# Performance work log

Measured on AMD Instinct MI355X. Metric: run time of the kernel, lower is better.

## Reference

```python
import jax, jax.numpy as jnp
import numpy as np

N_NODES = 8192
IN_F = 256
OUT_F = 256
ALPHA = 0.2  # LeakyReLU negative slope


def setup_inputs() -> dict:
    key = jax.random.key(0)
    k1, k2, k3, k4 = jax.random.split(key, 4)
    X = jax.random.normal(k1, (N_NODES, IN_F), dtype=jnp.float32)
    A = jax.random.randint(k2, (N_NODES, N_NODES), 0, 2, dtype=jnp.int32)
    # torch nn.Linear weight layout: (out_features, in_features)
    W = jax.random.normal(k3, (OUT_F, IN_F), dtype=jnp.float32) * (1.0 / np.sqrt(IN_F))
    r = jax.random.normal(k4, (2 * OUT_F, 1), dtype=jnp.float32)
    return {"X": X, "A": A, "W": W, "r": r}


def reference(X, A, W, r):
    # Wh = X @ W^T  -> (N, F_out)
    Wh = X @ W.T
    # Split r so that cat([Wh_i, Wh_j]) @ r == Wh_i @ r_src + Wh_j @ r_dst
    F_out = Wh.shape[-1]
    r_src = r[:F_out, 0]   # (F,)
    r_dst = r[F_out:, 0]   # (F,)
    s_i = Wh @ r_src       # (N,)
    s_j = Wh @ r_dst       # (N,)
    e = s_i[:, None] + s_j[None, :]                      # (N, N)
    e = jnp.where(e >= 0, e, ALPHA * e)                  # LeakyReLU
    e = jnp.where(A == 0, -jnp.inf, e)                   # mask non-edges
    attention = jax.nn.softmax(e, axis=1)                # row-wise softmax
    output = attention @ Wh                              # (N, F_out)
    return jax.nn.gelu(output, approximate=False)        # torch F.gelu (exact)
```

## Files before the change

kernel.cpp:

```cpp
#include <hip/hip_runtime.h>
#include <hip/hip_bf16.h>

#define N_NODES 8192
#define NF      256
#define L2E     1.44269504088896341f

typedef __attribute__((ext_vector_type(8))) short short8;
typedef __attribute__((ext_vector_type(4))) short short4v;
typedef __attribute__((ext_vector_type(4))) float floatx4;

static __device__ __forceinline__ float bf2f(short s) {
    return __uint_as_float(((unsigned)(unsigned short)s) << 16);
}
static __device__ __forceinline__ short f2bf_rn(float f) {
    unsigned u = __float_as_uint(f) + 0x8000u;
    return (short)(u >> 16);
}
struct bfpair { short hi, lo; };
static __device__ __forceinline__ bfpair split_bf(float x) {
    bfpair p;
    p.hi = f2bf_rn(x);
    p.lo = f2bf_rn(x - bf2f(p.hi));
    return p;
}
static __device__ __forceinline__ void async16(const void* g, void* l) {
    __builtin_amdgcn_global_load_lds(
        (const __attribute__((address_space(1))) unsigned*)g,
        (__attribute__((address_space(3))) unsigned*)l, 16, 0, 0);
}

__global__ __launch_bounds__(256) void kx_split(const float* __restrict__ W,
                                                short* __restrict__ Whi,
                                                short* __restrict__ Wlo) {
    #pragma unroll
    for (int e = 0; e < 4; ++e) {
        const int i = blockIdx.x * 1024 + e * 256 + threadIdx.x;
        bfpair p = split_bf(W[i]);
        Whi[i] = p.hi;
        Wlo[i] = p.lo;
    }
}

__global__ __launch_bounds__(512) void k1_gemm(const float* __restrict__ X,
                                               const short* __restrict__ Whi,
                                               const short* __restrict__ Wlo,
                                               const float* __restrict__ r,
                                               short* __restrict__ WhT,
                                               float* __restrict__ sp_src,
                                               float* __restrict__ sp_dst) {
    __shared__ float Xs[32 * 256];

    const int tid = threadIdx.x;
    const int w = tid >> 6, lane = tid & 63;
    const int q = lane >> 4, m = lane & 15;
    const int rh = w >> 2, cq = w & 3;
    const int i_base = blockIdx.x * 32;

    #pragma unroll
    for (int v = 0; v < 4; ++v) {
        const int rowv = w * 4 + v;
        const int c = lane ^ (rowv & 7);
        async16(X + (size_t)(i_base + rowv) * NF + c * 4, &Xs[rowv * 256]);
    }
    __syncthreads();

    floatx4 acc[4] = {};
    const int xrow = rh * 16 + m;
    const int r7 = xrow & 7;
    #pragma unroll
    for (int ks = 0; ks < 8; ++ks) {
        const int c0 = ks * 8 + q * 2;
        float4 f0 = *(const float4*)(&Xs[xrow * 256 + ((c0 ^ r7) * 4)]);
        float4 f1 = *(const float4*)(&Xs[xrow * 256 + (((c0 + 1) ^ r7) * 4)]);
        const float xsv[8] = {f0.x, f0.y, f0.z, f0.w, f1.x, f1.y, f1.z, f1.w};
        short8 xh, xl;
        #pragma unroll
        for (int c = 0; c < 8; ++c) {
            bfpair p = split_bf(xsv[c]);
            xh[c] = p.hi; xl[c] = p.lo;
        }
        #pragma unroll
        for (int nt = 0; nt < 4; ++nt) {
            const int n = cq * 64 + nt * 16 + m;
            short8 wh = *(const short8*)(Whi + n * NF + ks * 32 + q * 8);
            short8 wl = *(const short8*)(Wlo + n * NF + ks * 32 + q * 8);
            acc[nt] = __builtin_amdgcn_mfma_f32_16x16x32_bf16(xh, wh, acc[nt], 0, 0, 0);
            acc[nt] = __builtin_amdgcn_mfma_f32_16x16x32_bf16(xl, wh, acc[nt], 0, 0, 0);
            acc[nt] = __builtin_amdgcn_mfma_f32_16x16x32_bf16(xh, wl, acc[nt], 0, 0, 0);
        }
    }

    const int i0 = i_base + rh * 16 + q * 4;
    float vs[4] = {0.f, 0.f, 0.f, 0.f}, vd[4] = {0.f, 0.f, 0.f, 0.f};
    #pragma unroll
    for (int nt = 0; nt < 4; ++nt) {
        const int n = cq * 64 + nt * 16 + m;
        short4v v;
        #pragma unroll
        for (int r2 = 0; r2 < 4; ++r2) v[r2] = f2bf_rn(acc[nt][r2]);
        *(short4v*)(WhT + (size_t)n * N_NODES + i0) = v;
        const float rs = r[n], rd = r[NF + n];
        #pragma unroll
        for (int r2 = 0; r2 < 4; ++r2) {
            vs[r2] = fmaf(acc[nt][r2], rs, vs[r2]);
            vd[r2] = fmaf(acc[nt][r2], rd, vd[r2]);
        }
    }
    #pragma unroll
    for (int mask = 1; mask <= 8; mask <<= 1) {
        #pragma unroll
        for (int r2 = 0; r2 < 4; ++r2) {
            vs[r2] += __shfl_xor(vs[r2], mask);
            vd[r2] += __shfl_xor(vd[r2], mask);
        }
    }
    if (m == 0) {
        #pragma unroll
        for (int r2 = 0; r2 < 4; ++r2) {
            sp_src[cq * N_NODES + i0 + r2] = vs[r2];
            sp_dst[cq * N_NODES + i0 + r2] = vd[r2];
        }
    }
}

__global__ __launch_bounds__(256) void k2_sv(const float* __restrict__ sp_src,
                                             const float* __restrict__ sp_dst,
                                             float* __restrict__ s_src,
                                             float* __restrict__ s_dst,
                                             float* __restrict__ pmax) {
    __shared__ float red[256];
    const int tid = threadIdx.x;
    const int i = blockIdx.x * 256 + tid;
    float ss = 0.f, sd = 0.f;
    #pragma unroll
    for (int nb = 0; nb < 4; ++nb) {
        ss += sp_src[nb * N_NODES + i];
        sd += sp_dst[nb * N_NODES + i];
    }
    s_src[i] = ss;
    s_dst[i] = sd;
    red[tid] = sd;
    __syncthreads();
    for (int off = 128; off > 0; off >>= 1) {
        if (tid < off) red[tid] = fmaxf(red[tid], red[tid + off]);
        __syncthreads();
    }
    if (tid == 0) pmax[blockIdx.x] = red[0];
}

static __device__ __forceinline__ void pgroup(const int4 a, const floatx4 t,
                                              const float s_i, const float d_i,
                                              float* p) {
    const int av[4] = {a.x, a.y, a.z, a.w};
    #pragma unroll
    for (int c = 0; c < 4; ++c) {
        float sum = s_i + t[c];
        float lr  = fmaxf(sum, 0.2f * sum);
        float pp  = __builtin_amdgcn_exp2f(fmaf(lr, L2E, d_i));
        p[c] = (av[c] != 0) ? pp : 0.0f;
    }
}

__global__ __launch_bounds__(1024) void k4_attn(const int* __restrict__ Adj,
                                                const short* __restrict__ WhT,
                                                const float* __restrict__ s_dst,
                                                const float* __restrict__ s_src,
                                                const float* __restrict__ pmax,
                                                float* __restrict__ out) {
    __shared__ union {
        short B[4 * 256 * 64];
        float red[16 * 8 * 4 * 64];
    } sm;
    __shared__ float denred[128];

    const int tid = threadIdx.x;
    const int w = tid >> 6, lane = tid & 63;
    const int q = lane >> 4, m = lane & 15;
    const int rh = w >> 3, ch = (w >> 2) & 1, jq = w & 3;
    const int i0 = blockIdx.x * 32;
    const int row = i0 + rh * 16 + m;

    float M = pmax[0];
    #pragma unroll
    for (int b = 1; b < 32; ++b) M = fmaxf(M, pmax[b]);
    const float s_i = s_src[row];
    const float e0 = s_i + M;
    const float d_i = -fmaxf(e0, 0.2f * e0) * L2E;

    const int ug = w >> 2;
    const int jqs = w & 3;
    const int srow = lane >> 3;
    const int schunk = (lane & 7) ^ srow;
    const short* gB = WhT + (size_t)(ug * 64 + srow) * N_NODES + jqs * 64 + schunk * 8;
    short* ldsB = sm.B + (jqs * 256 + ug * 64) * 64;

    const int* Arow = Adj + (size_t)row * N_NODES + jq * 64 + q * 8;
    const float* tb = s_dst + jq * 64 + q * 8;

    floatx4 acc[8] = {{0.f,0.f,0.f,0.f}};
    #pragma unroll
    for (int nt = 0; nt < 8; ++nt) acc[nt] = (floatx4){0.f,0.f,0.f,0.f};
    float den = 0.f;

    #pragma unroll
    for (int v = 0; v < 8; ++v)
        async16(gB + v * 8 * N_NODES, ldsB + v * 8 * 64);
    int4 a0 = *(const int4*)(Arow);
    int4 a1 = *(const int4*)(Arow + 4);
    int4 a2 = *(const int4*)(Arow + 32);
    int4 a3 = *(const int4*)(Arow + 36);
    __syncthreads();

    for (int s = 0; s < 32; ++s) {
        const int offn = (s < 31) ? (s + 1) * 256 : s * 256;
        int4 na0 = *(const int4*)(Arow + offn);
        int4 na1 = *(const int4*)(Arow + offn + 4);
        int4 na2 = *(const int4*)(Arow + offn + 32);
        int4 na3 = *(const int4*)(Arow + offn + 36);
        const int ts = s * 256;
        floatx4 t0 = *(const floatx4*)(tb + ts);
        floatx4 t1 = *(const floatx4*)(tb + ts + 4);
        floatx4 t2 = *(const floatx4*)(tb + ts + 32);
        floatx4 t3 = *(const floatx4*)(tb + ts + 36);

        float p[16];
        pgroup(a0, t0, s_i, d_i, p);
        pgroup(a1, t1, s_i, d_i, p + 4);
        pgroup(a2, t2, s_i, d_i, p + 8);
        pgroup(a3, t3, s_i, d_i, p + 12);

        short8 af0, af1;
        #pragma unroll
        for (int c = 0; c < 8; ++c) { af0[c] = f2bf_rn(p[c]); af1[c] = f2bf_rn(p[8 + c]); }
        float ds = 0.f;
        #pragma unroll
        for (int c = 0; c < 16; ++c) ds += p[c];
        den += ds;

        const short* Bj = sm.B + jq * 256 * 64;
        #pragma unroll
        for (int nt = 0; nt < 8; ++nt) {
            const int n = ch * 128 + nt * 16 + m;
            const short* bp = Bj + n * 64;
            const int sw = n & 7;
            short8 b0 = *(const short8*)(bp + ((q ^ sw) * 8));
            short8 b1 = *(const short8*)(bp + (((q + 4) ^ sw) * 8));
            acc[nt] = __builtin_amdgcn_mfma_f32_16x16x32_bf16(af0, b0, acc[nt], 0, 0, 0);
            acc[nt] = __builtin_amdgcn_mfma_f32_16x16x32_bf16(af1, b1, acc[nt], 0, 0, 0);
        }
        a0 = na0; a1 = na1; a2 = na2; a3 = na3;

        __syncthreads();
        if (s < 31) {
            const int go = (s + 1) * 256;
            #pragma unroll
            for (int v = 0; v < 8; ++v)
                async16(gB + go + v * 8 * N_NODES, ldsB + v * 8 * 64);
            __syncthreads();
        }
    }

    den += __shfl_xor(den, 16);
    den += __shfl_xor(den, 32);
    if (ch == 0 && lane < 16) denred[rh * 64 + jq * 16 + lane] = den;
    #pragma unroll
    for (int nt = 0; nt < 8; ++nt)
        #pragma unroll
        for (int rg = 0; rg < 4; ++rg)
            sm.red[((w * 8 + nt) * 4 + rg) * 64 + lane] = acc[nt][rg];
    __syncthreads();

    float invd[4];
    #pragma unroll
    for (int rg = 0; rg < 4; ++rg) {
        const int rr = rh * 64 + q * 4 + rg;
        invd[rg] = 1.0f / fmaxf(denred[rr] + denred[rr + 16] +
                                denred[rr + 32] + denred[rr + 48], 1e-30f);
    }
    const int wb = rh * 8 + ch * 4;
    #pragma unroll
    for (int t2 = 0; t2 < 2; ++t2) {
        const int nt = jq * 2 + t2;
        #pragma unroll
        for (int rg = 0; rg < 4; ++rg) {
            float v = sm.red[(((wb + 0) * 8 + nt) * 4 + rg) * 64 + lane]
                    + sm.red[(((wb + 1) * 8 + nt) * 4 + rg) * 64 + lane]
                    + sm.red[(((wb + 2) * 8 + nt) * 4 + rg) * 64 + lane]
                    + sm.red[(((wb + 3) * 8 + nt) * 4 + rg) * 64 + lane];
            float x = v * invd[rg];
            float g = 0.5f * x * (1.0f + erff(x * 0.70710678118f));
            out[(size_t)(i0 + rh * 16 + q * 4 + rg) * NF + ch * 128 + nt * 16 + m] = g;
        }
    }
}

extern "C" void kernel_launch(void* const* d_in, const int* in_sizes, int n_in,
                              void* d_out, int out_size, void* d_ws, size_t ws_size,
                              hipStream_t stream) {
    const float* X = (const float*)d_in[0];
    const int*   A = (const int*)d_in[1];
    const float* W = (const float*)d_in[2];
    const float* r = (const float*)d_in[3];
    float* out = (float*)d_out;

    char* wsp = (char*)d_ws;
    short* WhT    = (short*)wsp;                    wsp += (size_t)NF * N_NODES * 2;
    short* Whi    = (short*)wsp;                    wsp += NF * NF * 2;
    short* Wlo    = (short*)wsp;                    wsp += NF * NF * 2;
    float* sp_src = (float*)wsp;                    wsp += 4 * N_NODES * 4;
    float* sp_dst = (float*)wsp;                    wsp += 4 * N_NODES * 4;
    float* s_src  = (float*)wsp;                    wsp += N_NODES * 4;
    float* s_dst  = (float*)wsp;                    wsp += N_NODES * 4;
    float* pmax   = (float*)wsp;

    kx_split<<<64, 256, 0, stream>>>(W, Whi, Wlo);
    k1_gemm<<<256, 512, 0, stream>>>(X, Whi, Wlo, r, WhT, sp_src, sp_dst);
    k2_sv<<<32, 256, 0, stream>>>(sp_src, sp_dst, s_src, s_dst, pmax);
    k4_attn<<<256, 1024, 0, stream>>>(A, WhT, s_dst, s_src, pmax, out);
}
```

Baseline: 481.7 us.

## Switch attention kernel to 32x32 MFMA with double-buffered Wh tiles

Restructures the attention-times-Wh kernel to use 32x32x16 bf16 MFMA tiles instead of 16x16x32, remapping waves so each covers all 32 rows and a 64-column slice of the output over a 32-wide slice of the key dimension. The Wh tile load changes from a single buffer of 256 columns to two 128-column LDS buffers. The next tile's async load is now issued before the current tile's compute, which removes one barrier per iteration and overlaps the load with the MFMAs. The epilogue reduction and denominator handling are rewritten to match the new fragment layout. The cost is twice as many loop iterations, each doing less work.

```diff
diff --git a/kernel.cpp b/kernel.cpp
--- a/kernel.cpp
+++ b/kernel.cpp
@@ -8,6 +8,7 @@
 typedef __attribute__((ext_vector_type(8))) short short8;
 typedef __attribute__((ext_vector_type(4))) short short4v;
 typedef __attribute__((ext_vector_type(4))) float floatx4;
+typedef __attribute__((ext_vector_type(16))) float floatx16;
 
 static __device__ __forceinline__ float bf2f(short s) {
     return __uint_as_float(((unsigned)(unsigned short)s) << 16);
@@ -168,17 +169,18 @@
                                                 const float* __restrict__ pmax,
                                                 float* __restrict__ out) {
     __shared__ union {
-        short B[4 * 256 * 64];
-        float red[16 * 8 * 4 * 64];
+        short B[2][256 * 128];
+        float red[32768];
     } sm;
-    __shared__ float denred[128];
+    __shared__ float denred[16 * 32];
+    __shared__ float invden[32];
 
     const int tid = threadIdx.x;
     const int w = tid >> 6, lane = tid & 63;
-    const int q = lane >> 4, m = lane & 15;
-    const int rh = w >> 3, ch = (w >> 2) & 1, jq = w & 3;
+    const int nq = w & 3, jg = w >> 2;
+    const int l31 = lane & 31, lh = lane >> 5, l15 = lane & 15;
     const int i0 = blockIdx.x * 32;
-    const int row = i0 + rh * 16 + m;
+    const int row = i0 + l31;
 
     float M = pmax[0];
     #pragma unroll
@@ -187,41 +189,58 @@
     const float e0 = s_i + M;
     const float d_i = -fmaxf(e0, 0.2f * e0) * L2E;
 
-    const int ug = w >> 2;
-    const int jqs = w & 3;
-    const int srow = lane >> 3;
-    const int schunk = (lane & 7) ^ srow;
-    const short* gB = WhT + (size_t)(ug * 64 + srow) * N_NODES + jqs * 64 + schunk * 8;
-    short* ldsB = sm.B + (jqs * 256 + ug * 64) * 64;
-
-    const int* Arow = Adj + (size_t)row * N_NODES + jq * 64 + q * 8;
-    const float* tb = s_dst + jq * 64 + q * 8;
-
-    floatx4 acc[8] = {{0.f,0.f,0.f,0.f}};
-    #pragma unroll
-    for (int nt = 0; nt < 8; ++nt) acc[nt] = (floatx4){0.f,0.f,0.f,0.f};
+    const short* gB[4];
+    #pragma unroll
+    for (int v = 0; v < 4; ++v) {
+        const int nlo = v * 4 + (lane >> 4);
+        const int c = l15 ^ nlo;
+        gB[v] = WhT + (size_t)(w * 16 + nlo) * N_NODES + c * 8;
+    }
+
+    const int jcA = jg * 4 + lh;
+    int boff0[2], boff1[2];
+    #pragma unroll
+    for (int nt = 0; nt < 2; ++nt) {
+        const int n = nq * 64 + nt * 32 + l31;
+        boff0[nt] = n * 128 + ((jcA ^ l15) * 8);
+        boff1[nt] = n * 128 + (((jcA + 2) ^ l15) * 8);
+    }
+
+    const int* aB = Adj + (size_t)row * N_NODES + jg * 32 + lh * 8;
+    const float* tB = s_dst + jg * 32 + lh * 8;
+
+    floatx16 acc0 = {}, acc1 = {};
     float den = 0.f;
 
     #pragma unroll
-    for (int v = 0; v < 8; ++v)
-        async16(gB + v * 8 * N_NODES, ldsB + v * 8 * 64);
-    int4 a0 = *(const int4*)(Arow);
-    int4 a1 = *(const int4*)(Arow + 4);
-    int4 a2 = *(const int4*)(Arow + 32);
-    int4 a3 = *(const int4*)(Arow + 36);
-    __syncthreads();
-
-    for (int s = 0; s < 32; ++s) {
-        const int offn = (s < 31) ? (s + 1) * 256 : s * 256;
-        int4 na0 = *(const int4*)(Arow + offn);
-        int4 na1 = *(const int4*)(Arow + offn + 4);
-        int4 na2 = *(const int4*)(Arow + offn + 32);
-        int4 na3 = *(const int4*)(Arow + offn + 36);
-        const int ts = s * 256;
-        floatx4 t0 = *(const floatx4*)(tb + ts);
-        floatx4 t1 = *(const floatx4*)(tb + ts + 4);
-        floatx4 t2 = *(const floatx4*)(tb + ts + 32);
-        floatx4 t3 = *(const floatx4*)(tb + ts + 36);
+    for (int v = 0; v < 4; ++v)
+        async16(gB[v], &sm.B[0][(w * 16 + v * 4) * 128]);
+    int4 a0 = *(const int4*)(aB);
+    int4 a1 = *(const int4*)(aB + 4);
+    int4 a2 = *(const int4*)(aB + 16);
+    int4 a3 = *(const int4*)(aB + 20);
+    __syncthreads();
+
+    for (int s = 0; s < 64; ++s) {
+        const short* Bc = sm.B[s & 1];
+        short* Bn = sm.B[(s & 1) ^ 1];
+
+        if (s < 63) {
+            const int jn = (s + 1) * 128;
+            #pragma unroll
+            for (int v = 0; v < 4; ++v)
+                async16(gB[v] + jn, Bn + (w * 16 + v * 4) * 128);
+        }
+        const int an = (s < 63) ? (s + 1) * 128 : s * 128;
+        int4 na0 = *(const int4*)(aB + an);
+        int4 na1 = *(const int4*)(aB + an + 4);
+        int4 na2 = *(const int4*)(aB + an + 16);
+        int4 na3 = *(const int4*)(aB + an + 20);
+        const float* tp = tB + s * 128;
+        floatx4 t0 = *(const floatx4*)(tp);
+        floatx4 t1 = *(const floatx4*)(tp + 4);
+        floatx4 t2 = *(const floatx4*)(tp + 16);
+        floatx4 t3 = *(const floatx4*)(tp + 20);
 
         float p[16];
         pgroup(a0, t0, s_i, d_i, p);
@@ -237,59 +256,64 @@
         for (int c = 0; c < 16; ++c) ds += p[c];
         den += ds;
 
-        const short* Bj = sm.B + jq * 256 * 64;
-        #pragma unroll
-        for (int nt = 0; nt < 8; ++nt) {
-            const int n = ch * 128 + nt * 16 + m;
-            const short* bp = Bj + n * 64;
-            const int sw = n & 7;
-            short8 b0 = *(const short8*)(bp + ((q ^ sw) * 8));
-            short8 b1 = *(const short8*)(bp + (((q + 4) ^ sw) * 8));
-            acc[nt] = __builtin_amdgcn_mfma_f32_16x16x32_bf16(af0, b0, acc[nt], 0, 0, 0);
-            acc[nt] = __builtin_amdgcn_mfma_f32_16x16x32_bf16(af1, b1, acc[nt], 0, 0, 0);
+        {
+            short8 b0 = *(const short8*)(Bc + boff0[0]);
+            short8 b1 = *(const short8*)(Bc + boff1[0]);
+            acc0 = __builtin_amdgcn_mfma_f32_32x32x16_bf16(af0, b0, acc0, 0, 0, 0);
+            acc0 = __builtin_amdgcn_mfma_f32_32x32x16_bf16(af1, b1, acc0, 0, 0, 0);
+        }
+        {
+            short8 b0 = *(const short8*)(Bc + boff0[1]);
+            short8 b1 = *(const short8*)(Bc + boff1[1]);
+            acc1 = __builtin_amdgcn_mfma_f32_32x32x16_bf16(af0, b0, acc1, 0, 0, 0);
+            acc1 = __builtin_amdgcn_mfma_f32_32x32x16_bf16(af1, b1, acc1, 0, 0, 0);
         }
         a0 = na0; a1 = na1; a2 = na2; a3 = na3;
 
         __syncthreads();
-        if (s < 31) {
-            const int go = (s + 1) * 256;
-            #pragma unroll
-            for (int v = 0; v < 8; ++v)
-                async16(gB + go + v * 8 * N_NODES, ldsB + v * 8 * 64);
-            __syncthreads();
-        }
-    }
-
-    den += __shfl_xor(den, 16);
+    }
+
     den += __shfl_xor(den, 32);
-    if (ch == 0 && lane < 16) denred[rh * 64 + jq * 16 + lane] = den;
-    #pragma unroll
-    for (int nt = 0; nt < 8; ++nt)
-        #pragma unroll
-        for (int rg = 0; rg < 4; ++rg)
-            sm.red[((w * 8 + nt) * 4 + rg) * 64 + lane] = acc[nt][rg];
-    __syncthreads();
-
-    float invd[4];
-    #pragma unroll
-    for (int rg = 0; rg < 4; ++rg) {
-        const int rr = rh * 64 + q * 4 + rg;
-        invd[rg] = 1.0f / fmaxf(denred[rr] + denred[rr + 16] +
-                                denred[rr + 32] + denred[rr + 48], 1e-30f);
-    }
-    const int wb = rh * 8 + ch * 4;
-    #pragma unroll
-    for (int t2 = 0; t2 < 2; ++t2) {
-        const int nt = jq * 2 + t2;
-        #pragma unroll
-        for (int rg = 0; rg < 4; ++rg) {
-            float v = sm.red[(((wb + 0) * 8 + nt) * 4 + rg) * 64 + lane]
-                    + sm.red[(((wb + 1) * 8 + nt) * 4 + rg) * 64 + lane]
-                    + sm.red[(((wb + 2) * 8 + nt) * 4 + rg) * 64 + lane]
-                    + sm.red[(((wb + 3) * 8 + nt) * 4 + rg) * 64 + lane];
-            float x = v * invd[rg];
+    if (lane < 32) denred[w * 32 + lane] = den;
+    __syncthreads();
+    if (tid < 32) {
+        float d = 0.f;
+        #pragma unroll
+        for (int u = 0; u < 4; ++u) d += denred[(u * 4) * 32 + tid];
+        invden[tid] = 1.0f / fmaxf(d, 1e-30f);
+    }
+
+    #pragma unroll
+    for (int rq = 0; rq < 4; ++rq) {
+        float4 v0, v1;
+        v0.x = acc0[rq * 4 + 0]; v0.y = acc0[rq * 4 + 1];
+        v0.z = acc0[rq * 4 + 2]; v0.w = acc0[rq * 4 + 3];
+        v1.x = acc1[rq * 4 + 0]; v1.y = acc1[rq * 4 + 1];
+        v1.z = acc1[rq * 4 + 2]; v1.w = acc1[rq * 4 + 3];
+        *(float4*)(&sm.red[(((w * 2 + 0) * 4 + rq) * 64 + lane) * 4]) = v0;
+        *(float4*)(&sm.red[(((w * 2 + 1) * 4 + rq) * 64 + lane) * 4]) = v1;
+    }
+    __syncthreads();
+
+    const int ntw = jg & 1;
+    #pragma unroll
+    for (int h = 0; h < 2; ++h) {
+        const int rq = (jg >> 1) + h * 2;
+        float4 v = {0.f, 0.f, 0.f, 0.f};
+        #pragma unroll
+        for (int jg2 = 0; jg2 < 4; ++jg2) {
+            const int wp = jg2 * 4 + nq;
+            float4 u = *(const float4*)(&sm.red[(((wp * 2 + ntw) * 4 + rq) * 64 + lane) * 4]);
+            v.x += u.x; v.y += u.y; v.z += u.z; v.w += u.w;
+        }
+        const int n = nq * 64 + ntw * 32 + l31;
+        const float vv[4] = {v.x, v.y, v.z, v.w};
+        #pragma unroll
+        for (int t = 0; t < 4; ++t) {
+            const int rrow = t + 8 * rq + 4 * lh;
+            float x = vv[t] * invden[rrow];
             float g = 0.5f * x * (1.0f + erff(x * 0.70710678118f));
-            out[(size_t)(i0 + rh * 16 + q * 4 + rg) * NF + ch * 128 + nt * 16 + m] = g;
+            out[(size_t)(i0 + rrow) * NF + n] = g;
         }
     }
 }
```

New measurement: 563.0 us. 1.17x slower.

## Split attention over two column halves with 32x32 MFMA and separate GELU epilogue

Applied to the files above, without the earlier changes.

The attention kernel now runs 512 blocks of 512 threads, each handling 32 rows over half of the neighbour columns. It uses 32x32x16 bf16 MFMAs with a smaller 128-column LDS tile and no register prefetch of adjacency. Partial numerators and denominators go to workspace, and a new kernel combines the two halves, normalizes and applies GELU. The goal is better occupancy and MFMA efficiency. The cost is an extra launch, about 16 MB of partial-sum traffic, and loss of load/compute overlap because the adjacency prefetch and double-step pipelining were removed.

```diff
diff --git a/kernel.cpp b/kernel.cpp
--- a/kernel.cpp
+++ b/kernel.cpp
@@ -8,6 +8,7 @@
 typedef __attribute__((ext_vector_type(8))) short short8;
 typedef __attribute__((ext_vector_type(4))) short short4v;
 typedef __attribute__((ext_vector_type(4))) float floatx4;
+typedef __attribute__((ext_vector_type(16))) float floatx16;
 
 static __device__ __forceinline__ float bf2f(short s) {
     return __uint_as_float(((unsigned)(unsigned short)s) << 16);
@@ -161,24 +162,27 @@
     }
 }
 
-__global__ __launch_bounds__(1024) void k4_attn(const int* __restrict__ Adj,
-                                                const short* __restrict__ WhT,
-                                                const float* __restrict__ s_dst,
-                                                const float* __restrict__ s_src,
-                                                const float* __restrict__ pmax,
-                                                float* __restrict__ out) {
+__global__ __launch_bounds__(512, 4) void k4_attn(const int* __restrict__ Adj,
+                                                  const short* __restrict__ WhT,
+                                                  const float* __restrict__ s_dst,
+                                                  const float* __restrict__ s_src,
+                                                  const float* __restrict__ pmax,
+                                                  float* __restrict__ nump,
+                                                  float* __restrict__ denp) {
     __shared__ union {
-        short B[4 * 256 * 64];
-        float red[16 * 8 * 4 * 64];
+        short B[256 * 128];
+        float red[8 * 16 * 64];
     } sm;
-    __shared__ float denred[128];
+    __shared__ float denred[4 * 32];
 
     const int tid = threadIdx.x;
     const int w = tid >> 6, lane = tid & 63;
-    const int q = lane >> 4, m = lane & 15;
-    const int rh = w >> 3, ch = (w >> 2) & 1, jq = w & 3;
-    const int i0 = blockIdx.x * 32;
-    const int row = i0 + rh * 16 + m;
+    const int jq = w & 3, nh = w >> 2;
+    const int l31 = lane & 31, lh = lane >> 5, l15 = lane & 15;
+    const int ib = (int)blockIdx.x >> 1, jh = (int)blockIdx.x & 1;
+    const int i0 = ib * 32;
+    const int row = i0 + l31;
+    const int jbase = jh * 4096;
 
     float M = pmax[0];
     #pragma unroll
@@ -187,41 +191,42 @@
     const float e0 = s_i + M;
     const float d_i = -fmaxf(e0, 0.2f * e0) * L2E;
 
-    const int ug = w >> 2;
-    const int jqs = w & 3;
-    const int srow = lane >> 3;
-    const int schunk = (lane & 7) ^ srow;
-    const short* gB = WhT + (size_t)(ug * 64 + srow) * N_NODES + jqs * 64 + schunk * 8;
-    short* ldsB = sm.B + (jqs * 256 + ug * 64) * 64;
-
-    const int* Arow = Adj + (size_t)row * N_NODES + jq * 64 + q * 8;
-    const float* tb = s_dst + jq * 64 + q * 8;
-
-    floatx4 acc[8] = {{0.f,0.f,0.f,0.f}};
-    #pragma unroll
-    for (int nt = 0; nt < 8; ++nt) acc[nt] = (floatx4){0.f,0.f,0.f,0.f};
+    int voff[8];
+    #pragma unroll
+    for (int v = 0; v < 8; ++v) {
+        const int n = w * 32 + v * 4 + (lane >> 4);
+        const int c = l15 ^ (n & 15);
+        voff[v] = n * N_NODES + c * 8;
+    }
+    const short* gBbase = WhT + jbase;
+
+    const int slot0 = (jq * 4 + lh) ^ l15;
+    const int slot1 = (jq * 4 + 2 + lh) ^ l15;
+    const int nrow = nh * 128 + l31;
+    const int boffA = nrow * 128 + slot0 * 8;
+    const int boffB = nrow * 128 + slot1 * 8;
+
+    const int* aPtr = Adj + (size_t)row * N_NODES + jbase + jq * 32 + lh * 8;
+    const float* tPtr = s_dst + jbase + jq * 32 + lh * 8;
+
+    floatx16 acc[4] = {};
     float den = 0.f;
 
-    #pragma unroll
-    for (int v = 0; v < 8; ++v)
-        async16(gB + v * 8 * N_NODES, ldsB + v * 8 * 64);
-    int4 a0 = *(const int4*)(Arow);
-    int4 a1 = *(const int4*)(Arow + 4);
-    int4 a2 = *(const int4*)(Arow + 32);
-    int4 a3 = *(const int4*)(Arow + 36);
-    __syncthreads();
-
     for (int s = 0; s < 32; ++s) {
-        const int offn = (s < 31) ? (s + 1) * 256 : s * 256;
-        int4 na0 = *(const int4*)(Arow + offn);
-        int4 na1 = *(const int4*)(Arow + offn + 4);
-        int4 na2 = *(const int4*)(Arow + offn + 32);
-        int4 na3 = *(const int4*)(Arow + offn + 36);
-        const int ts = s * 256;
-        floatx4 t0 = *(const floatx4*)(tb + ts);
-        floatx4 t1 = *(const floatx4*)(tb + ts + 4);
-        floatx4 t2 = *(const floatx4*)(tb + ts + 32);
-        floatx4 t3 = *(const floatx4*)(tb + ts + 36);
+        const int jo = s * 128;
+        #pragma unroll
+        for (int v = 0; v < 8; ++v)
+            async16(gBbase + jo + voff[v], sm.B + (w * 32 + v * 4) * 128);
+        __syncthreads();
+
+        int4 a0 = *(const int4*)(aPtr + jo);
+        int4 a1 = *(const int4*)(aPtr + jo + 4);
+        int4 a2 = *(const int4*)(aPtr + jo + 16);
+        int4 a3 = *(const int4*)(aPtr + jo + 20);
+        floatx4 t0 = *(const floatx4*)(tPtr + jo);
+        floatx4 t1 = *(const floatx4*)(tPtr + jo + 4);
+        floatx4 t2 = *(const floatx4*)(tPtr + jo + 16);
+        floatx4 t3 = *(const floatx4*)(tPtr + jo + 20);
 
         float p[16];
         pgroup(a0, t0, s_i, d_i, p);
@@ -237,61 +242,56 @@
         for (int c = 0; c < 16; ++c) ds += p[c];
         den += ds;
 
-        const short* Bj = sm.B + jq * 256 * 64;
-        #pragma unroll
-        for (int nt = 0; nt < 8; ++nt) {
-            const int n = ch * 128 + nt * 16 + m;
-            const short* bp = Bj + n * 64;
-            const int sw = n & 7;
-            short8 b0 = *(const short8*)(bp + ((q ^ sw) * 8));
-            short8 b1 = *(const short8*)(bp + (((q + 4) ^ sw) * 8));
-            acc[nt] = __builtin_amdgcn_mfma_f32_16x16x32_bf16(af0, b0, acc[nt], 0, 0, 0);
-            acc[nt] = __builtin_amdgcn_mfma_f32_16x16x32_bf16(af1, b1, acc[nt], 0, 0, 0);
-        }
-        a0 = na0; a1 = na1; a2 = na2; a3 = na3;
-
-        __syncthreads();
-        if (s < 31) {
-            const int go = (s + 1) * 256;
-            #pragma unroll
-            for (int v = 0; v < 8; ++v)
-                async16(gB + go + v * 8 * N_NODES, ldsB + v * 8 * 64);
-            __syncthreads();
-        }
-    }
-
-    den += __shfl_xor(den, 16);
+        #pragma unroll
+        for (int nt = 0; nt < 4; ++nt) {
+            short8 b0 = *(const short8*)(sm.B + boffA + nt * 4096);
+            short8 b1 = *(const short8*)(sm.B + boffB + nt * 4096);
+            acc[nt] = __builtin_amdgcn_mfma_f32_32x32x16_bf16(af0, b0, acc[nt], 0, 0, 0);
+            acc[nt] = __builtin_amdgcn_mfma_f32_32x32x16_bf16(af1, b1, acc[nt], 0, 0, 0);
+        }
+        __syncthreads();
+    }
+
     den += __shfl_xor(den, 32);
-    if (ch == 0 && lane < 16) denred[rh * 64 + jq * 16 + lane] = den;
-    #pragma unroll
-    for (int nt = 0; nt < 8; ++nt)
-        #pragma unroll
-        for (int rg = 0; rg < 4; ++rg)
-            sm.red[((w * 8 + nt) * 4 + rg) * 64 + lane] = acc[nt][rg];
-    __syncthreads();
-
-    float invd[4];
-    #pragma unroll
-    for (int rg = 0; rg < 4; ++rg) {
-        const int rr = rh * 64 + q * 4 + rg;
-        invd[rg] = 1.0f / fmaxf(denred[rr] + denred[rr + 16] +
-                                denred[rr + 32] + denred[rr + 48], 1e-30f);
-    }
-    const int wb = rh * 8 + ch * 4;
-    #pragma unroll
-    for (int t2 = 0; t2 < 2; ++t2) {
-        const int nt = jq * 2 + t2;
-        #pragma unroll
-        for (int rg = 0; rg < 4; ++rg) {
-            float v = sm.red[(((wb + 0) * 8 + nt) * 4 + rg) * 64 + lane]
-                    + sm.red[(((wb + 1) * 8 + nt) * 4 + rg) * 64 + lane]
-                    + sm.red[(((wb + 2) * 8 + nt) * 4 + rg) * 64 + lane]
-                    + sm.red[(((wb + 3) * 8 + nt) * 4 + rg) * 64 + lane];
-            float x = v * invd[rg];
-            float g = 0.5f * x * (1.0f + erff(x * 0.70710678118f));
-            out[(size_t)(i0 + rh * 16 + q * 4 + rg) * NF + ch * 128 + nt * 16 + m] = g;
-        }
-    }
+    if (w < 4 && lane < 32) denred[w * 32 + lane] = den;
+
+    float* numq = nump + (size_t)jh * N_NODES * NF;
+    #pragma unroll
+    for (int nt = 0; nt < 4; ++nt) {
+        #pragma unroll
+        for (int rg = 0; rg < 16; ++rg)
+            sm.red[(w * 16 + rg) * 64 + lane] = acc[nt][rg];
+        __syncthreads();
+        if (nt == 0 && tid < 32) {
+            float d = denred[tid] + denred[32 + tid] + denred[64 + tid] + denred[96 + tid];
+            denp[jh * N_NODES + i0 + tid] = d;
+        }
+        const int nh2 = w & 1;
+        const int rb = (w >> 1) * 4;
+        #pragma unroll
+        for (int k = 0; k < 4; ++k) {
+            const int rg = rb + k;
+            float v = sm.red[((nh2 * 4 + 0) * 16 + rg) * 64 + lane]
+                    + sm.red[((nh2 * 4 + 1) * 16 + rg) * 64 + lane]
+                    + sm.red[((nh2 * 4 + 2) * 16 + rg) * 64 + lane]
+                    + sm.red[((nh2 * 4 + 3) * 16 + rg) * 64 + lane];
+            const int rrow = (rg & 3) + 8 * (rg >> 2) + 4 * lh;
+            const int nn = nh2 * 128 + nt * 32 + l31;
+            numq[(size_t)(i0 + rrow) * NF + nn] = v;
+        }
+        __syncthreads();
+    }
+}
+
+__global__ __launch_bounds__(256) void k5_out(const float* __restrict__ nump,
+                                              const float* __restrict__ denp,
+                                              float* __restrict__ out) {
+    const int idx = blockIdx.x * 256 + threadIdx.x;
+    const int i = idx >> 8;
+    float num = nump[idx] + nump[N_NODES * NF + idx];
+    float den = denp[i] + denp[N_NODES + i];
+    float x = num / fmaxf(den, 1e-30f);
+    out[idx] = 0.5f * x * (1.0f + erff(x * 0.70710678118f));
 }
 
 extern "C" void kernel_launch(void* const* d_in, const int* in_sizes, int n_in,
@@ -311,10 +311,13 @@
     float* sp_dst = (float*)wsp;                    wsp += 4 * N_NODES * 4;
     float* s_src  = (float*)wsp;                    wsp += N_NODES * 4;
     float* s_dst  = (float*)wsp;                    wsp += N_NODES * 4;
-    float* pmax   = (float*)wsp;
+    float* pmax   = (float*)wsp;                    wsp += 32 * 4;
+    float* denp   = (float*)wsp;                    wsp += 2 * N_NODES * 4;
+    float* nump   = (float*)wsp;
 
     kx_split<<<64, 256, 0, stream>>>(W, Whi, Wlo);
     k1_gemm<<<256, 512, 0, stream>>>(X, Whi, Wlo, r, WhT, sp_src, sp_dst);
     k2_sv<<<32, 256, 0, stream>>>(sp_src, sp_dst, s_src, s_dst, pmax);
-    k4_attn<<<256, 1024, 0, stream>>>(A, WhT, s_dst, s_src, pmax, out);
-}
+    k4_attn<<<512, 512, 0, stream>>>(A, WhT, s_dst, s_src, pmax, nump, denp);
+    k5_out<<<N_NODES * NF / 256, 256, 0, stream>>>(nump, denp, out);
+}
```

Result: slower. 495.5 us (+2.9%).
